# Kernel optimization log

Hardware: AMD Instinct MI355X
Metric: run time of the kernel (lower is better)

The kernel has to match this reference:

```python
import jax, jax.numpy as jnp
import numpy as np

EPS = 1e-12  # F.normalize default eps

def _l2norm(x):
    return x / jnp.maximum(jnp.linalg.norm(x, axis=-1, keepdims=True), EPS)

def setup_inputs() -> dict:
    key = jax.random.key(0)
    k1, k2, k3 = jax.random.split(key, 3)
    N, C, D = 131072, 1000, 256
    feat = jax.random.normal(k1, (N, D), dtype=jnp.float32)
    # memory bank is initialized to L2-normalized centers in the original (init())
    memory = _l2norm(jax.random.normal(k2, (C, D), dtype=jnp.float32))
    label = jax.random.randint(k3, (N,), 0, C, dtype=jnp.int64)
    return {"feat": feat, "memory": memory, "label": label}

def reference(feat, memory, label):
    num_cls, feat_dim = memory.shape
    N = feat.shape[0]
    t = 1.0  # forward default temperature

    featn = _l2norm(feat)

    # --- update(feat, label): fused per-class masked gather+sum as one segment_sum ---
    f = jax.lax.stop_gradient(featn)  # feat.detach() in original
    sums = jax.ops.segment_sum(f, label, num_segments=num_cls)          # [C, D]
    counts = jax.ops.segment_sum(jnp.ones((N,), f.dtype), label, num_segments=num_cls)
    flags = (counts > 0).astype(f.dtype)[:, None]                        # [C, 1]
    batch_center = _l2norm(sums) * flags                                 # zeros for empty classes

    # --- update_center_by_simi ---
    simi = jnp.sum(memory * batch_center, axis=-1, keepdims=True)        # [C, 1]
    update_wei = 1.0 - (1.0 - simi) * flags                              # [C, 1]
    new_memory = _l2norm(update_wei * memory + (1.0 - update_wei) * batch_center)

    # --- similarity + cross entropy ---
    simis = jnp.einsum('nd,cd->nc', featn, new_memory) / t               # [N, C]
    logp = jax.nn.log_softmax(simis, axis=-1)
    loss = -jnp.mean(jnp.take_along_axis(logp, label[:, None], axis=1))
    return loss
```

## Files before the change

kernel.cpp:

```cpp
#include <hip/hip_runtime.h>
#include <hip/hip_fp8.h>

#define NROWS 131072
#define NCLS  1000
#define CPAD  1024
#define DDIM  256

typedef __attribute__((ext_vector_type(4))) float f32x4;
typedef __attribute__((ext_vector_type(2))) long l64x2;

__device__ __forceinline__ float wred(float v){
#pragma unroll
  for (int m = 1; m < 64; m <<= 1) v += __shfl_xor(v, m, 64);
  return v;
}

__device__ __forceinline__ float fexp2(float x){
#if __has_builtin(__builtin_amdgcn_exp2f)
  return __builtin_amdgcn_exp2f(x);
#else
  float r; asm("v_exp_f32 %0, %1" : "=v"(r) : "v"(x)); return r;
#endif
}

__device__ __forceinline__ unsigned pk4_fp8(float a, float b, float c, float d){
#if __has_builtin(__builtin_amdgcn_cvt_pk_fp8_f32)
  int v = __builtin_amdgcn_cvt_pk_fp8_f32(a, b, 0, false);
  v = __builtin_amdgcn_cvt_pk_fp8_f32(c, d, v, true);
  return (unsigned)v;
#else
  __hip_fp8_e4m3 fa(a), fb(b), fc(c), fd(d);
  return (unsigned)fa.__x | ((unsigned)fb.__x<<8) |
         ((unsigned)fc.__x<<16) | ((unsigned)fd.__x<<24);
#endif
}

__device__ __forceinline__ void store_frag8(unsigned char* nmem, int c, int ln,
                                            float a, float b, float x, float y){
  int c2 = c >> 4, r16c = c & 15;
  int k = ln >> 3, g = (ln >> 1) & 3, q = ln & 1;
  *(unsigned*)(nmem + c2*4096 + (k>>1)*1024 + (g*16+r16c)*16 + (k&1)*8 + q*4) =
      pk4_fp8(a, b, x, y);
}

__global__ __launch_bounds__(1024) void k_center(
    const float* __restrict__ feat, const float* __restrict__ memory,
    const int* __restrict__ label, unsigned char* __restrict__ nmem,
    float* __restrict__ nmemf32){
  const int c0 = blockIdx.x * 2;
  const int t = threadIdx.x;
  const int w = t >> 6, lane = t & 63;
  if (c0 >= NCLS){
    if (t < 128) store_frag8(nmem, c0 + (t >> 6), t & 63, 0.f, 0.f, 0.f, 0.f);
    return;
  }
  const int c1 = c0 + 1;
  __shared__ float4 accred[2][16][64];
  __shared__ int cw[2][16];

  float4 a0 = make_float4(0.f,0.f,0.f,0.f);
  float4 a1 = make_float4(0.f,0.f,0.f,0.f);
  int cnt0 = 0, cnt1 = 0;
  const float4* feat4 = (const float4*)feat;
  const int4*   lab4  = (const int4*)label;

  for (int it = 0; it < 32; ++it){
    int base = (w*32 + it) * 256;
    int4 lv = lab4[base/4 + lane];
#pragma unroll
    for (int sub = 0; sub < 4; ++sub){
      int lvv = (sub==0)?lv.x:(sub==1)?lv.y:(sub==2)?lv.z:lv.w;
      unsigned long long m0 = __ballot(lvv == c0);
      unsigned long long m1 = __ballot(lvv == c1);
      cnt0 += (int)__popcll(m0); cnt1 += (int)__popcll(m1);
      while (m0){
        int b = __ffsll((long long)m0) - 1; m0 &= m0 - 1;
        int r = base + b*4 + sub;
        float4 x = feat4[r*64 + lane];
        float ss = wred(x.x*x.x + x.y*x.y + x.z*x.z + x.w*x.w);
        float sc = 1.0f / fmaxf(sqrtf(ss), 1e-12f);
        a0.x += x.x*sc; a0.y += x.y*sc; a0.z += x.z*sc; a0.w += x.w*sc;
      }
      while (m1){
        int b = __ffsll((long long)m1) - 1; m1 &= m1 - 1;
        int r = base + b*4 + sub;
        float4 x = feat4[r*64 + lane];
        float ss = wred(x.x*x.x + x.y*x.y + x.z*x.z + x.w*x.w);
        float sc = 1.0f / fmaxf(sqrtf(ss), 1e-12f);
        a1.x += x.x*sc; a1.y += x.y*sc; a1.z += x.z*sc; a1.w += x.w*sc;
      }
    }
  }
  accred[0][w][lane] = a0; accred[1][w][lane] = a1;
  if (lane == 0){ cw[0][w] = cnt0; cw[1][w] = cnt1; }
  __syncthreads();

  if (t < 128){
    int cls = t >> 6, ln = t & 63;
    float sx=0.f, sy=0.f, sz=0.f, sw=0.f; int total = 0;
#pragma unroll
    for (int s = 0; s < 16; ++s){
      float4 v = accred[cls][s][ln];
      sx += v.x; sy += v.y; sz += v.z; sw += v.w;
      total += cw[cls][s];
    }
    int c = c0 + cls;
    float ss = wred(sx*sx + sy*sy + sz*sz + sw*sw);
    float inv = 1.0f / fmaxf(sqrtf(ss), 1e-12f);
    float bx = sx*inv, by = sy*inv, bz = sz*inv, bw = sw*inv;
    float flag = (total > 0) ? 1.0f : 0.0f;
    float4 m = ((const float4*)memory)[c*64 + ln];
    float simi = wred(m.x*bx + m.y*by + m.z*bz + m.w*bw);
    float wei = 1.0f - (1.0f - simi)*flag;
    float rx = wei*m.x + (1.0f-wei)*bx;
    float ry = wei*m.y + (1.0f-wei)*by;
    float rz = wei*m.z + (1.0f-wei)*bz;
    float rw = wei*m.w + (1.0f-wei)*bw;
    float ss2 = wred(rx*rx + ry*ry + rz*rz + rw*rw);
    float inv2 = 1.0f / fmaxf(sqrtf(ss2), 1e-12f);
    store_frag8(nmem, c, ln, rx*inv2, ry*inv2, rz*inv2, rw*inv2);
    ((float4*)nmemf32)[c*64 + ln] =
        make_float4(rx*inv2, ry*inv2, rz*inv2, rw*inv2);
  }
}

#define MFMA8 __builtin_amdgcn_mfma_f32_16x16x32_fp8_fp8

__global__ __launch_bounds__(256, 2) void k_gemm(
    const float* __restrict__ feat, const unsigned char* __restrict__ nmem,
    const float* __restrict__ nmemf32, const int* __restrict__ label,
    float* __restrict__ partials){
  __shared__ float bred[4];
  const int t = threadIdx.x, w = t >> 6, lane = t & 63;
  const int g = lane >> 4, r16 = lane & 15;
  const int rowbase = blockIdx.x * 128;

  long areg[2][8];
  float slabv[2];
#pragma unroll
  for (int mf = 0; mf < 2; ++mf){
    int row = rowbase + w*32 + mf*16 + r16;
    const float4* rp = (const float4*)(feat + row*DDIM);
    float ss = 0.f;
#pragma unroll
    for (int kt = 0; kt < 8; ++kt){
      float4 x0 = rp[kt*8 + g*2];
      float4 x1 = rp[kt*8 + g*2 + 1];
      ss += x0.x*x0.x + x0.y*x0.y + x0.z*x0.z + x0.w*x0.w
          + x1.x*x1.x + x1.y*x1.y + x1.z*x1.z + x1.w*x1.w;
    }
    ss += __shfl_xor(ss, 16, 64);
    ss += __shfl_xor(ss, 32, 64);
    float invn = 1.0f / fmaxf(sqrtf(ss), 1e-12f);
    float sc = 1.44269504f * invn;
    int lab = label[row];
    const float4* bp4 = (const float4*)(nmemf32 + (size_t)lab*DDIM);
    float dl = 0.f;
#pragma unroll
    for (int kt = 0; kt < 8; ++kt){
      float4 x0 = rp[kt*8 + g*2];
      float4 x1 = rp[kt*8 + g*2 + 1];
      float4 b0 = bp4[kt*8 + g*2];
      float4 b1 = bp4[kt*8 + g*2 + 1];
      unsigned lo = pk4_fp8(x0.x*sc, x0.y*sc, x0.z*sc, x0.w*sc);
      unsigned hi = pk4_fp8(x1.x*sc, x1.y*sc, x1.z*sc, x1.w*sc);
      areg[mf][kt] = (long)(((unsigned long)hi << 32) | lo);
      dl += x0.x*b0.x + x0.y*b0.y + x0.z*b0.z + x0.w*b0.w
          + x1.x*b1.x + x1.y*b1.y + x1.z*b1.z + x1.w*b1.w;
    }
    dl += __shfl_xor(dl, 16, 64);
    dl += __shfl_xor(dl, 32, 64);
    slabv[mf] = dl * invn;
  }
  float slab_epi[2][4];
#pragma unroll
  for (int m = 0; m < 2; ++m)
#pragma unroll
    for (int j = 0; j < 4; ++j)
      slab_epi[m][j] = __shfl(slabv[m], g*4 + j, 16);

  float esum[2][4] = {{0.f,0.f,0.f,0.f},{0.f,0.f,0.f,0.f}};

  const char* nbp = (const char*)nmem + lane*16;
  const int rot = blockIdx.x & 63;
  long b0[8], b1[8], b2[8];

#define LOADC(BUF, C)                                                         \
  { const char* cb = nbp + (size_t)(((C) + rot) & 63)*4096;                   \
    _Pragma("unroll")                                                         \
    for (int k2 = 0; k2 < 4; ++k2){                                           \
      l64x2 v = *(const l64x2*)(cb + k2*1024);                                \
      BUF[k2*2] = v.x; BUF[k2*2+1] = v.y; } }

#define BODY(CUR, PF, CIDX)                                                   \
  {                                                                           \
    if ((CIDX) + 2 < 64) LOADC(PF, (CIDX)+2);           \
    f32x4 a0_, a1_;                                                           \
    __builtin_amdgcn_s_setprio(1);                                            \
    { f32x4 Z = {0.f,0.f,0.f,0.f};                                            \
      a0_ = MFMA8(areg[0][0], CUR[0], Z, 0, 0, 0);                            \
      a1_ = MFMA8(areg[1][0], CUR[0], Z, 0, 0, 0); }                          \
    _Pragma("unroll")                                                         \
    for (int k = 1; k < 8; ++k){                                              \
      a0_ = MFMA8(areg[0][k], CUR[k], a0_, 0, 0, 0);                          \
      a1_ = MFMA8(areg[1][k], CUR[k], a1_, 0, 0, 0);                          \
    }                                                                         \
    __builtin_amdgcn_s_setprio(0);                                            \
    _Pragma("unroll")                                                         \
    for (int j = 0; j < 4; ++j){                                              \
      esum[0][j] += fexp2(a0_[j]);                                            \
      esum[1][j] += fexp2(a1_[j]);                                            \
    }                                                                         \
  }

  LOADC(b0, 0);
  LOADC(b1, 1);

  for (int p = 0; p < 21; ++p){
    int c = 3*p;
    BODY(b0, b2, c);
    BODY(b1, b0, c+1);
    BODY(b2, b1, c+2);
  }
  BODY(b0, b1, 63);

  float v = 0.f;
#pragma unroll
  for (int m = 0; m < 2; ++m)
#pragma unroll
    for (int j = 0; j < 4; ++j){
      float e = esum[m][j];
      e += __shfl_xor(e, 1, 64); e += __shfl_xor(e, 2, 64);
      e += __shfl_xor(e, 4, 64); e += __shfl_xor(e, 8, 64);
      v += 0.69314718056f * __log2f(e - 24.0f) - slab_epi[m][j];
    }
  if (r16 != 0) v = 0.f;
  v = wred(v);
  if (lane == 0) bred[w] = v;
  __syncthreads();
  if (t == 0) partials[blockIdx.x] = bred[0] + bred[1] + bred[2] + bred[3];
}

__global__ __launch_bounds__(256) void k_final(
    const float* __restrict__ partials, float* __restrict__ out){
  const int t = threadIdx.x;
  const int w = t >> 6, lane = t & 63;
  __shared__ float red[4];
  float s = partials[t] + partials[t+256] + partials[t+512] + partials[t+768];
  s = wred(s);
  if (lane == 0) red[w] = s;
  __syncthreads();
  if (t == 0) out[0] = (red[0]+red[1]+red[2]+red[3]) * (1.0f/(float)NROWS);
}

extern "C" void kernel_launch(void* const* d_in, const int* in_sizes, int n_in,
                              void* d_out, int out_size, void* d_ws, size_t ws_size,
                              hipStream_t stream){
  const float* feat   = (const float*)d_in[0];
  const float* memory = (const float*)d_in[1];
  const int*   label  = (const int*)d_in[2];
  float* out = (float*)d_out;
  unsigned char* nmem = (unsigned char*)d_ws;
  float* nmemf32 = (float*)((char*)d_ws + 262144);
  float* partials = (float*)((char*)d_ws + 1310720);

  k_center<<<CPAD/2, 1024, 0, stream>>>(feat, memory, label, nmem, nmemf32);
  k_gemm<<<NROWS/128, 256, 0, stream>>>(feat, nmem, nmemf32, label, partials);
  k_final<<<1, 256, 0, stream>>>(partials, out);
}
```

Measured before the change: 113.4 us.

## Switch FP8 GEMM to scaled 16x16x128 MFMA with repacked fragment layout

Replaces the chained 16x16x32 fp8 MFMAs (8 per tile) with the MI355 scaled 16x16x128 f8f6f4 MFMA using unit scales (2 per tile). The fragment layout of the fp8 memory bank and the A-register packing are rearranged so each lane holds 32 contiguous fp8 values per K-half. This is meant to raise matrix throughput and cut instruction issue, at the cost of larger register fragments and a new packing layout that must match exactly.

```diff
diff --git a/kernel.cpp b/kernel.cpp
--- a/kernel.cpp
+++ b/kernel.cpp
@@ -7,7 +7,10 @@
 #define DDIM  256
 
 typedef __attribute__((ext_vector_type(4))) float f32x4;
-typedef __attribute__((ext_vector_type(2))) long l64x2;
+typedef __attribute__((ext_vector_type(4))) int   i32x4;
+typedef __attribute__((ext_vector_type(8))) int   i32x8;
+
+#define SC1 0x7F7F7F7Fu
 
 __device__ __forceinline__ float wred(float v){
 #pragma unroll
@@ -38,8 +41,9 @@
 __device__ __forceinline__ void store_frag8(unsigned char* nmem, int c, int ln,
                                             float a, float b, float x, float y){
   int c2 = c >> 4, r16c = c & 15;
-  int k = ln >> 3, g = (ln >> 1) & 3, q = ln & 1;
-  *(unsigned*)(nmem + c2*4096 + (k>>1)*1024 + (g*16+r16c)*16 + (k&1)*8 + q*4) =
+  int d = ln*4, kh = d >> 7, rem = d & 127, g = rem >> 5, o = rem & 31;
+  int h = o >> 4, o4 = o & 15;
+  *(unsigned*)(nmem + c2*4096 + kh*2048 + h*1024 + (g*16+r16c)*16 + o4) =
       pk4_fp8(a, b, x, y);
 }
 
@@ -124,7 +128,8 @@
   }
 }
 
-#define MFMA8 __builtin_amdgcn_mfma_f32_16x16x32_fp8_fp8
+#define MFMAS(A, B, C) \
+  __builtin_amdgcn_mfma_scale_f32_16x16x128_f8f6f4((A), (B), (C), 0, 0, 0, SC1, 0, SC1)
 
 __global__ __launch_bounds__(256, 2) void k_gemm(
     const float* __restrict__ feat, const unsigned char* __restrict__ nmem,
@@ -135,7 +140,7 @@
   const int g = lane >> 4, r16 = lane & 15;
   const int rowbase = blockIdx.x * 128;
 
-  long areg[2][8];
+  i32x8 areg[2][2];
   float slabv[2];
 #pragma unroll
   for (int mf = 0; mf < 2; ++mf){
@@ -157,16 +162,16 @@
     const float4* bp4 = (const float4*)(nmemf32 + (size_t)lab*DDIM);
     float dl = 0.f;
 #pragma unroll
-    for (int kt = 0; kt < 8; ++kt){
-      float4 x0 = rp[kt*8 + g*2];
-      float4 x1 = rp[kt*8 + g*2 + 1];
-      float4 b0 = bp4[kt*8 + g*2];
-      float4 b1 = bp4[kt*8 + g*2 + 1];
-      unsigned lo = pk4_fp8(x0.x*sc, x0.y*sc, x0.z*sc, x0.w*sc);
-      unsigned hi = pk4_fp8(x1.x*sc, x1.y*sc, x1.z*sc, x1.w*sc);
-      areg[mf][kt] = (long)(((unsigned long)hi << 32) | lo);
-      dl += x0.x*b0.x + x0.y*b0.y + x0.z*b0.z + x0.w*b0.w
-          + x1.x*b1.x + x1.y*b1.y + x1.z*b1.z + x1.w*b1.w;
+    for (int kh = 0; kh < 2; ++kh){
+      i32x8 pk;
+#pragma unroll
+      for (int q = 0; q < 8; ++q){
+        float4 x = rp[kh*32 + g*8 + q];
+        float4 b = bp4[kh*32 + g*8 + q];
+        pk[q] = (int)pk4_fp8(x.x*sc, x.y*sc, x.z*sc, x.w*sc);
+        dl += x.x*b.x + x.y*b.y + x.z*b.z + x.w*b.w;
+      }
+      areg[mf][kh] = pk;
     }
     dl += __shfl_xor(dl, 16, 64);
     dl += __shfl_xor(dl, 32, 64);
@@ -183,14 +188,17 @@
 
   const char* nbp = (const char*)nmem + lane*16;
   const int rot = blockIdx.x & 63;
-  long b0[8], b1[8], b2[8];
+  i32x8 b0[2], b1[2], b2[2];
 
 #define LOADC(BUF, C)                                                         \
   { const char* cb = nbp + (size_t)(((C) + rot) & 63)*4096;                   \
     _Pragma("unroll")                                                         \
-    for (int k2 = 0; k2 < 4; ++k2){                                           \
-      l64x2 v = *(const l64x2*)(cb + k2*1024);                                \
-      BUF[k2*2] = v.x; BUF[k2*2+1] = v.y; } }
+    for (int kh = 0; kh < 2; ++kh){                                           \
+      i32x4 v0 = *(const i32x4*)(cb + kh*2048);                               \
+      i32x4 v1 = *(const i32x4*)(cb + kh*2048 + 1024);                        \
+      BUF[kh][0]=v0[0]; BUF[kh][1]=v0[1]; BUF[kh][2]=v0[2]; BUF[kh][3]=v0[3]; \
+      BUF[kh][4]=v1[0]; BUF[kh][5]=v1[1]; BUF[kh][6]=v1[2]; BUF[kh][7]=v1[3]; \
+    } }
 
 #define BODY(CUR, PF, CIDX)                                                   \
   {                                                                           \
@@ -198,13 +206,10 @@
     f32x4 a0_, a1_;                                                           \
     __builtin_amdgcn_s_setprio(1);                                            \
     { f32x4 Z = {0.f,0.f,0.f,0.f};                                            \
-      a0_ = MFMA8(areg[0][0], CUR[0], Z, 0, 0, 0);                            \
-      a1_ = MFMA8(areg[1][0], CUR[0], Z, 0, 0, 0); }                          \
-    _Pragma("unroll")                                                         \
-    for (int k = 1; k < 8; ++k){                                              \
-      a0_ = MFMA8(areg[0][k], CUR[k], a0_, 0, 0, 0);                          \
-      a1_ = MFMA8(areg[1][k], CUR[k], a1_, 0, 0, 0);                          \
-    }                                                                         \
+      a0_ = MFMAS(areg[0][0], CUR[0], Z);                                     \
+      a1_ = MFMAS(areg[1][0], CUR[0], Z); }                                   \
+    a0_ = MFMAS(areg[0][1], CUR[1], a0_);                                     \
+    a1_ = MFMAS(areg[1][1], CUR[1], a1_);                                     \
     __builtin_amdgcn_s_setprio(0);                                            \
     _Pragma("unroll")                                                         \
     for (int j = 0; j < 4; ++j){                                              \
```

Result: slower. 135.0 us (+19.0%).
